# Kernel tuning notes

Hardware: AMD Instinct MI355X
Metric: run time of the kernel (lower is better)

## Reference

```python
import jax, jax.numpy as jnp
import numpy as np

N, E, B = 200000, 6400000, 128
IN_LOCAL, IN_GLOBAL, HIDDEN, NUM_CLASSES = 16, 8, 32, 2


def setup_inputs() -> dict:
    key = jax.random.key(0)
    ks = jax.random.split(key, 16)
    inp = {
        "x_local": jax.random.normal(ks[0], (N, IN_LOCAL), dtype=jnp.float32),
        "x_global": jax.random.normal(ks[1], (B, IN_GLOBAL), dtype=jnp.float32),
        "batch": jnp.sort(jax.random.randint(ks[2], (N,), 0, B, dtype=jnp.int64)),
        "edge_index": jax.random.randint(ks[3], (2, E), 0, N, dtype=jnp.int64),
        # encoder params
        "W_local": jax.random.normal(ks[4], (IN_LOCAL, HIDDEN), jnp.float32) / np.sqrt(IN_LOCAL),
        "b_local": jnp.zeros((HIDDEN,), jnp.float32),
        "W_global": jax.random.normal(ks[5], (IN_GLOBAL, HIDDEN), jnp.float32) / np.sqrt(IN_GLOBAL),
        "b_global": jnp.zeros((HIDDEN,), jnp.float32),
        "W_mix": jax.random.normal(ks[6], (3 * HIDDEN, HIDDEN), jnp.float32) / np.sqrt(3 * HIDDEN),
        "b_mix": jnp.zeros((HIDDEN,), jnp.float32),
        # GNN layer params
        "W_msg": jax.random.normal(ks[7], (HIDDEN, HIDDEN), jnp.float32) / np.sqrt(HIDDEN),
        "b_msg": jnp.zeros((HIDDEN,), jnp.float32),
        "W_self": jax.random.normal(ks[8], (HIDDEN, HIDDEN), jnp.float32) / np.sqrt(HIDDEN),
        "b_self": jnp.zeros((HIDDEN,), jnp.float32),
        # output head
        "W_out": jax.random.normal(ks[9], (HIDDEN, NUM_CLASSES), jnp.float32) / np.sqrt(HIDDEN),
        "b_out": jnp.zeros((NUM_CLASSES,), jnp.float32),
    }
    return inp


def reference(x_local, x_global, batch, edge_index,
              W_local, b_local, W_global, b_global, W_mix, b_mix,
              W_msg, b_msg, W_self, b_self, W_out, b_out):
    n = x_local.shape[0]
    # --- MixedSelectivityNodeEncoder ---
    h_local = jax.nn.relu(x_local @ W_local + b_local)            # [N,H]
    h_global_graph = jax.nn.relu(x_global @ W_global + b_global)  # [B,H]
    h_global = h_global_graph[batch]                              # gather -> [N,H]
    h_int = h_local * h_global
    h_cat = jnp.concatenate([h_local, h_global, h_int], axis=-1)  # [N,3H]
    h0 = jax.nn.relu(h_cat @ W_mix + b_mix)                       # [N,H]
    # --- GNN layer with self loops, add aggregation ---
    loops = jnp.arange(n, dtype=edge_index.dtype)
    src = jnp.concatenate([edge_index[0], loops])                 # [E+N]
    dst = jnp.concatenate([edge_index[1], loops])                 # [E+N]
    msg = jax.nn.relu(h0[src] @ W_msg + b_msg)                    # [E+N,H]
    aggr = jax.ops.segment_sum(msg, dst, num_segments=n)          # [N,H]
    h = jax.nn.relu(aggr + h0 @ W_self + b_self)                  # [N,H]
    # --- output head ---
    return h @ W_out + b_out                                      # [N,C]
```

## Files before the change

### kernel.cpp

```cpp
#include <hip/hip_runtime.h>

#define N_NODES  200000
#define N_EDGES  6400000
#define NGRAPH   128
#define H        32

#define BNODES   256
#define NBUCK    782
#define P_BLOCKS 256
#define EPB      25000
#define SORT_CAP 10240

typedef unsigned short ushort_t;

__device__ __forceinline__ ushort_t f32_to_bf16_rne(float f) {
    unsigned u = __float_as_uint(f);
    unsigned r = (u + 0x7fffu + ((u >> 16) & 1u)) >> 16;
    return (ushort_t)r;
}
__device__ __forceinline__ float bf16_to_f32(ushort_t h) {
    return __uint_as_float(((unsigned)h) << 16);
}

__global__ __launch_bounds__(256) void k_node_enc(
        const float* __restrict__ xl,
        const int*   __restrict__ batch,
        const float* __restrict__ xg,   const float* __restrict__ Wg,
        const float* __restrict__ bg,
        const float* __restrict__ Wl,   const float* __restrict__ bl,
        const float* __restrict__ Wmix, const float* __restrict__ bmix,
        const float* __restrict__ Wmsg, const float* __restrict__ bmsg,
        const float* __restrict__ Wself,const float* __restrict__ bself,
        ushort_t* __restrict__ mb, float* __restrict__ s) {
    int n0 = blockIdx.x * 256 + threadIdx.x;
    bool valid = (n0 < N_NODES);
    int n = valid ? n0 : (N_NODES - 1);

    float xv[16];
    {
        const float4* p = (const float4*)(xl + (size_t)n * 16);
        float4 a = p[0], b = p[1], c = p[2], d = p[3];
        xv[0]=a.x; xv[1]=a.y; xv[2]=a.z; xv[3]=a.w;
        xv[4]=b.x; xv[5]=b.y; xv[6]=b.z; xv[7]=b.w;
        xv[8]=c.x; xv[9]=c.y; xv[10]=c.z; xv[11]=c.w;
        xv[12]=d.x; xv[13]=d.y; xv[14]=d.z; xv[15]=d.w;
    }
    float gvv[8];
    {
        int gb = batch[n];
        const float4* q = (const float4*)(xg + (size_t)gb * 8);
        float4 a = q[0], b = q[1];
        gvv[0]=a.x; gvv[1]=a.y; gvv[2]=a.z; gvv[3]=a.w;
        gvv[4]=b.x; gvv[5]=b.y; gvv[6]=b.z; gvv[7]=b.w;
    }

    float hl[32], hg[32], hi[32];
#pragma unroll
    for (int t4 = 0; t4 < 8; ++t4) {
        float4 al = ((const float4*)bl)[t4];
        float4 ag = ((const float4*)bg)[t4];
#pragma unroll
        for (int k = 0; k < 16; ++k) {
            float4 w = ((const float4*)(Wl + k * H))[t4];
            al.x = fmaf(xv[k], w.x, al.x); al.y = fmaf(xv[k], w.y, al.y);
            al.z = fmaf(xv[k], w.z, al.z); al.w = fmaf(xv[k], w.w, al.w);
        }
#pragma unroll
        for (int k = 0; k < 8; ++k) {
            float4 w = ((const float4*)(Wg + k * H))[t4];
            ag.x = fmaf(gvv[k], w.x, ag.x); ag.y = fmaf(gvv[k], w.y, ag.y);
            ag.z = fmaf(gvv[k], w.z, ag.z); ag.w = fmaf(gvv[k], w.w, ag.w);
        }
        hl[t4*4+0] = fmaxf(al.x, 0.f); hl[t4*4+1] = fmaxf(al.y, 0.f);
        hl[t4*4+2] = fmaxf(al.z, 0.f); hl[t4*4+3] = fmaxf(al.w, 0.f);
        hg[t4*4+0] = fmaxf(ag.x, 0.f); hg[t4*4+1] = fmaxf(ag.y, 0.f);
        hg[t4*4+2] = fmaxf(ag.z, 0.f); hg[t4*4+3] = fmaxf(ag.w, 0.f);
    }
#pragma unroll
    for (int k = 0; k < 32; ++k) hi[k] = hl[k] * hg[k];

    float h0[32];
#pragma unroll
    for (int t4 = 0; t4 < 8; ++t4) {
        float4 acc = ((const float4*)bmix)[t4];
#pragma unroll
        for (int k = 0; k < 32; ++k) {
            float4 w = ((const float4*)(Wmix + k * H))[t4];
            acc.x = fmaf(hl[k], w.x, acc.x); acc.y = fmaf(hl[k], w.y, acc.y);
            acc.z = fmaf(hl[k], w.z, acc.z); acc.w = fmaf(hl[k], w.w, acc.w);
        }
#pragma unroll
        for (int k = 0; k < 32; ++k) {
            float4 w = ((const float4*)(Wmix + (32 + k) * H))[t4];
            acc.x = fmaf(hg[k], w.x, acc.x); acc.y = fmaf(hg[k], w.y, acc.y);
            acc.z = fmaf(hg[k], w.z, acc.z); acc.w = fmaf(hg[k], w.w, acc.w);
        }
#pragma unroll
        for (int k = 0; k < 32; ++k) {
            float4 w = ((const float4*)(Wmix + (64 + k) * H))[t4];
            acc.x = fmaf(hi[k], w.x, acc.x); acc.y = fmaf(hi[k], w.y, acc.y);
            acc.z = fmaf(hi[k], w.z, acc.z); acc.w = fmaf(hi[k], w.w, acc.w);
        }
        h0[t4*4+0] = fmaxf(acc.x, 0.f); h0[t4*4+1] = fmaxf(acc.y, 0.f);
        h0[t4*4+2] = fmaxf(acc.z, 0.f); h0[t4*4+3] = fmaxf(acc.w, 0.f);
    }

#pragma unroll
    for (int t4 = 0; t4 < 8; ++t4) {
        float4 am = ((const float4*)bmsg)[t4];
        float4 as = ((const float4*)bself)[t4];
#pragma unroll
        for (int k = 0; k < 32; ++k) {
            float4 wm = ((const float4*)(Wmsg + k * H))[t4];
            float4 ws = ((const float4*)(Wself + k * H))[t4];
            am.x = fmaf(h0[k], wm.x, am.x); am.y = fmaf(h0[k], wm.y, am.y);
            am.z = fmaf(h0[k], wm.z, am.z); am.w = fmaf(h0[k], wm.w, am.w);
            as.x = fmaf(h0[k], ws.x, as.x); as.y = fmaf(h0[k], ws.y, as.y);
            as.z = fmaf(h0[k], ws.z, as.z); as.w = fmaf(h0[k], ws.w, as.w);
        }
        if (valid) {
            unsigned d0 = (unsigned)f32_to_bf16_rne(fmaxf(am.x, 0.f))
                        | ((unsigned)f32_to_bf16_rne(fmaxf(am.y, 0.f)) << 16);
            unsigned d1 = (unsigned)f32_to_bf16_rne(fmaxf(am.z, 0.f))
                        | ((unsigned)f32_to_bf16_rne(fmaxf(am.w, 0.f)) << 16);
            ((unsigned*)(mb + (size_t)n * H))[t4*2+0] = d0;
            ((unsigned*)(mb + (size_t)n * H))[t4*2+1] = d1;
            ((float4*)(s + (size_t)n * H))[t4] = as;
        }
    }
}

__global__ __launch_bounds__(1024) void k_pcount(const int* __restrict__ ei,
                                                 int* __restrict__ gcnt) {
    __shared__ int cnt[NBUCK];
    int t = threadIdx.x, blk = blockIdx.x;
    for (int i = t; i < NBUCK; i += 1024) cnt[i] = 0;
    __syncthreads();
    int e1 = (blk + 1) * EPB;
    for (int e = blk * EPB + t; e < e1; e += 1024)
        atomicAdd(&cnt[ei[N_EDGES + e] >> 8], 1);
    __syncthreads();
    for (int i = t; i < NBUCK; i += 1024)
        gcnt[i * P_BLOCKS + blk] = cnt[i];
}

__global__ void k_blocksum_g(const int* __restrict__ gcnt, int* __restrict__ bsum) {
    int b = blockIdx.x, t = threadIdx.x;
    int v = gcnt[b * P_BLOCKS + t];
#pragma unroll
    for (int off = 32; off >= 1; off >>= 1)
        v += __shfl_down(v, off, 64);
    __shared__ int w4[4];
    if ((t & 63) == 0) w4[t >> 6] = v;
    __syncthreads();
    if (t == 0) bsum[b] = w4[0] + w4[1] + w4[2] + w4[3];
}

__global__ void k_scan_bsums_g(const int* __restrict__ bsum, int* __restrict__ boff) {
    __shared__ int sd[1024];
    int t = threadIdx.x;
    sd[t] = (t < NBUCK) ? bsum[t] : 0;
    __syncthreads();
#pragma unroll
    for (int off = 1; off < 1024; off <<= 1) {
        int v = (t >= off) ? sd[t - off] : 0;
        __syncthreads();
        sd[t] += v;
        __syncthreads();
    }
    if (t < NBUCK) boff[t] = (t == 0) ? 0 : sd[t - 1];
}

__global__ void k_make_cursor_g(int* __restrict__ gcnt, const int* __restrict__ boff) {
    __shared__ int sd[P_BLOCKS];
    int b = blockIdx.x, t = threadIdx.x, i = b * P_BLOCKS + t;
    int c = gcnt[i];
    sd[t] = c;
    __syncthreads();
#pragma unroll
    for (int off = 1; off < P_BLOCKS; off <<= 1) {
        int v = (t >= off) ? sd[t - off] : 0;
        __syncthreads();
        sd[t] += v;
        __syncthreads();
    }
    gcnt[i] = boff[b] + sd[t] - c;
}

__global__ __launch_bounds__(1024) void k_pscatter(const int* __restrict__ ei,
                                                   const int* __restrict__ goff,
                                                   unsigned int* __restrict__ ebuf) {
    __shared__ int cur[NBUCK];
    int t = threadIdx.x, blk = blockIdx.x;
    for (int i = t; i < NBUCK; i += 1024) cur[i] = goff[i * P_BLOCKS + blk];
    __syncthreads();
    int e1 = (blk + 1) * EPB;
    for (int e = blk * EPB + t; e < e1; e += 1024) {
        unsigned src = (unsigned)ei[e];
        int dst = ei[N_EDGES + e];
        int pos = atomicAdd(&cur[dst >> 8], 1);
        ebuf[pos] = (src << 8) | (unsigned)(dst & 255);
    }
}

__global__ __launch_bounds__(512) void k_bsort_aggr(
        const int* __restrict__ goff,
        const unsigned int* __restrict__ ebuf,
        const ushort_t* __restrict__ mb, const float* __restrict__ s,
        const float* __restrict__ Wout, const float* __restrict__ bout,
        float* __restrict__ out) {
    __shared__ unsigned sorted[SORT_CAP];
    __shared__ int cnt[BNODES];
    __shared__ int off[BNODES];
    __shared__ int cur[BNODES];
    int tid = threadIdx.x, b = blockIdx.x;

    int bs = goff[b * P_BLOCKS];
    int be = (b == NBUCK - 1) ? N_EDGES : goff[(b + 1) * P_BLOCKS];

    if (tid < BNODES) cnt[tid] = 0;
    __syncthreads();

    for (int j = bs + tid; j < be; j += 512)
        atomicAdd(&cnt[ebuf[j] & 255], 1);
    __syncthreads();

    if (tid < BNODES) off[tid] = cnt[tid];
    __syncthreads();
#pragma unroll
    for (int d = 1; d < BNODES; d <<= 1) {
        int v = (tid < BNODES && tid >= d) ? off[tid - d] : 0;
        __syncthreads();
        if (tid < BNODES) off[tid] += v;
        __syncthreads();
    }
    if (tid < BNODES) cur[tid] = off[tid] - cnt[tid];
    __syncthreads();

    for (int j = bs + tid; j < be; j += 512) {
        unsigned pk = ebuf[j];
        int pos = atomicAdd(&cur[pk & 255], 1);
        sorted[pos] = pk;
    }
    __syncthreads();

    const unsigned* mb32 = (const unsigned*)mb;
    int g = tid >> 4;
    int t = tid & 15;

    for (int q = 0; q < 8; ++q) {
        int loc = (g << 3) + q;
        int n = b * BNODES + loc;
        int rs = off[loc] - cnt[loc];
        int re = off[loc];
        float a0 = 0.f, a1 = 0.f;

        for (int j = rs; j < re; j += 8) {
            unsigned pk[8], u[8];
#pragma unroll
            for (int k = 0; k < 8; ++k)
                pk[k] = sorted[min(j + k, re - 1)];
#pragma unroll
            for (int k = 0; k < 8; ++k)
                u[k] = mb32[(pk[k] >> 8) * 16u + (unsigned)t];
#pragma unroll
            for (int k = 0; k < 8; ++k) {
                bool ok = (j + k < re);
                a0 += ok ? __uint_as_float(u[k] << 16)         : 0.f;
                a1 += ok ? __uint_as_float(u[k] & 0xffff0000u) : 0.f;
            }
        }

        if (n < N_NODES) {
            unsigned u = mb32[(unsigned)n * 16u + (unsigned)t];
            float2 sv = *(const float2*)(s + (size_t)n * H + 2 * t);
            float h0 = fmaxf(a0 + __uint_as_float(u << 16)         + sv.x, 0.f);
            float h1 = fmaxf(a1 + __uint_as_float(u & 0xffff0000u) + sv.y, 0.f);
            float4 w = *(const float4*)(Wout + 4 * t);
            float p0 = h0 * w.x + h1 * w.z;
            float p1 = h0 * w.y + h1 * w.w;
#pragma unroll
            for (int o = 8; o >= 1; o >>= 1) {
                p0 += __shfl_down(p0, o, 16);
                p1 += __shfl_down(p1, o, 16);
            }
            if (t == 0) {
                float2 o2;
                o2.x = p0 + bout[0];
                o2.y = p1 + bout[1];
                *(float2*)(out + (size_t)n * 2) = o2;
            }
        }
    }
}

extern "C" void kernel_launch(void* const* d_in, const int* in_sizes, int n_in,
                              void* d_out, int out_size, void* d_ws, size_t ws_size,
                              hipStream_t stream) {
    const float* xl    = (const float*)d_in[0];
    const float* xg    = (const float*)d_in[1];
    const int*   batch = (const int*)  d_in[2];
    const int*   ei    = (const int*)  d_in[3];
    const float* Wl    = (const float*)d_in[4];
    const float* bl    = (const float*)d_in[5];
    const float* Wg    = (const float*)d_in[6];
    const float* bg    = (const float*)d_in[7];
    const float* Wmix  = (const float*)d_in[8];
    const float* bmix  = (const float*)d_in[9];
    const float* Wmsg  = (const float*)d_in[10];
    const float* bmsg  = (const float*)d_in[11];
    const float* Wself = (const float*)d_in[12];
    const float* bself = (const float*)d_in[13];
    const float* Wout  = (const float*)d_in[14];
    const float* bout  = (const float*)d_in[15];
    float* out = (float*)d_out;

    float*    s    = (float*)d_ws;
    ushort_t* mb   = (ushort_t*)(s + (size_t)N_NODES * H);
    int*      gcnt = (int*)(mb + (size_t)N_NODES * H);
    int*      bsum = gcnt + (size_t)NBUCK * P_BLOCKS;
    int*      boff = bsum + NBUCK;
    unsigned int* ebuf = (unsigned int*)(boff + NBUCK);

    k_node_enc<<<(N_NODES + 255) / 256, 256, 0, stream>>>(xl, batch, xg, Wg, bg,
                                                          Wl, bl, Wmix, bmix,
                                                          Wmsg, bmsg, Wself, bself,
                                                          mb, s);

    k_pcount<<<P_BLOCKS, 1024, 0, stream>>>(ei, gcnt);
    k_blocksum_g<<<NBUCK, P_BLOCKS, 0, stream>>>(gcnt, bsum);
    k_scan_bsums_g<<<1, 1024, 0, stream>>>(bsum, boff);
    k_make_cursor_g<<<NBUCK, P_BLOCKS, 0, stream>>>(gcnt, boff);
    k_pscatter<<<P_BLOCKS, 1024, 0, stream>>>(ei, gcnt, ebuf);

    k_bsort_aggr<<<NBUCK, 512, 0, stream>>>(gcnt, ebuf, mb, s, Wout, bout, out);
}
```

Measured before the change: 389.1 us.

## Scatter edges into fixed-capacity per-bucket slots with global atomics, skipping count/scan passes

Replaces the count, block-sum, scan, cursor and partitioned-scatter pipeline with a single scatter kernel. It uses padded global atomic counters per bucket and writes into fixed SORT_CAP slots per bucket, removing a full read pass over edge_index and several launches. The aggregation kernel's in-block prefix scan now uses wavefront shuffles instead of a shared-memory Hillis-Steele loop, and SORT_CAP is reduced to allow more occupancy. Edges past SORT_CAP in a bucket are silently dropped, and global atomic contention on the 782 counters may cost throughput. The old path is kept as a fallback when the workspace is too small.

```diff
diff --git a/kernel.cpp b/kernel.cpp
--- a/kernel.cpp
+++ b/kernel.cpp
@@ -9,7 +9,8 @@
 #define NBUCK    782
 #define P_BLOCKS 256
 #define EPB      25000
-#define SORT_CAP 10240
+#define SORT_CAP 8960
+
 
 typedef unsigned short ushort_t;
 
@@ -203,42 +204,80 @@
     }
 }
 
-__global__ __launch_bounds__(512) void k_bsort_aggr(
+__global__ __launch_bounds__(256) void k_pscatter_direct(
+        const int* __restrict__ ei,
+        int* __restrict__ gcur,
+        unsigned int* __restrict__ ebuf) {
+    int e = blockIdx.x * 256 + threadIdx.x;
+    int stride = gridDim.x * 256;
+    for (; e < N_EDGES; e += stride) {
+        unsigned src = (unsigned)ei[e];
+        int dst = ei[N_EDGES + e];
+        int bkt = dst >> 8;
+        int pos = atomicAdd(&gcur[bkt * 32], 1);
+        if (pos < SORT_CAP)
+            ebuf[(size_t)bkt * SORT_CAP + pos] = (src << 8) | (unsigned)(dst & 255);
+    }
+}
+
+__global__ __launch_bounds__(512, 8) void k_bsort_aggr(
         const int* __restrict__ goff,
+        const int* __restrict__ gcur,
+        int mode,
         const unsigned int* __restrict__ ebuf,
         const ushort_t* __restrict__ mb, const float* __restrict__ s,
         const float* __restrict__ Wout, const float* __restrict__ bout,
         float* __restrict__ out) {
     __shared__ unsigned sorted[SORT_CAP];
     __shared__ int cnt[BNODES];
-    __shared__ int off[BNODES];
+    __shared__ int offx[BNODES + 1];
     __shared__ int cur[BNODES];
+    __shared__ int wsum[4];
     int tid = threadIdx.x, b = blockIdx.x;
 
-    int bs = goff[b * P_BLOCKS];
-    int be = (b == NBUCK - 1) ? N_EDGES : goff[(b + 1) * P_BLOCKS];
+    size_t base;
+    int sz;
+    if (mode) {
+        base = (size_t)b * SORT_CAP;
+        sz = min(gcur[b * 32], SORT_CAP);
+    } else {
+        int bs = goff[b * P_BLOCKS];
+        int be = (b == NBUCK - 1) ? N_EDGES : goff[(b + 1) * P_BLOCKS];
+        base = (size_t)bs;
+        sz = be - bs;
+    }
 
     if (tid < BNODES) cnt[tid] = 0;
     __syncthreads();
 
-    for (int j = bs + tid; j < be; j += 512)
-        atomicAdd(&cnt[ebuf[j] & 255], 1);
-    __syncthreads();
-
-    if (tid < BNODES) off[tid] = cnt[tid];
-    __syncthreads();
-#pragma unroll
-    for (int d = 1; d < BNODES; d <<= 1) {
-        int v = (tid < BNODES && tid >= d) ? off[tid - d] : 0;
-        __syncthreads();
-        if (tid < BNODES) off[tid] += v;
-        __syncthreads();
-    }
-    if (tid < BNODES) cur[tid] = off[tid] - cnt[tid];
-    __syncthreads();
-
-    for (int j = bs + tid; j < be; j += 512) {
-        unsigned pk = ebuf[j];
+    for (int j = tid; j < sz; j += 512)
+        atomicAdd(&cnt[ebuf[base + j] & 255], 1);
+    __syncthreads();
+
+    {
+        int lane = tid & 63, w = tid >> 6;
+        int v = (tid < BNODES) ? cnt[tid] : 0;
+#pragma unroll
+        for (int d = 1; d < 64; d <<= 1) {
+            int u = __shfl_up(v, d, 64);
+            if (lane >= d) v += u;
+        }
+        if (tid < BNODES && lane == 63) wsum[w] = v;
+        __syncthreads();
+        if (tid < BNODES) {
+            int add = 0;
+#pragma unroll
+            for (int i = 0; i < 3; ++i) add += (i < w) ? wsum[i] : 0;
+            int inc = v + add;
+            offx[tid + 1] = inc;
+            cur[tid] = inc - cnt[tid];
+            if (tid == 0) offx[0] = 0;
+        }
+        __syncthreads();
+    }
+
+    for (int j = tid; j < sz; j += 512) {
+        unsigned pk = ebuf[base + j];
         int pos = atomicAdd(&cur[pk & 255], 1);
         sorted[pos] = pk;
     }
@@ -251,8 +290,8 @@
     for (int q = 0; q < 8; ++q) {
         int loc = (g << 3) + q;
         int n = b * BNODES + loc;
-        int rs = off[loc] - cnt[loc];
-        int re = off[loc];
+        int rs = offx[loc];
+        int re = offx[loc + 1];
         float a0 = 0.f, a1 = 0.f;
 
         for (int j = rs; j < re; j += 8) {
@@ -315,23 +354,38 @@
     const float* bout  = (const float*)d_in[15];
     float* out = (float*)d_out;
 
-    float*    s    = (float*)d_ws;
-    ushort_t* mb   = (ushort_t*)(s + (size_t)N_NODES * H);
-    int*      gcnt = (int*)(mb + (size_t)N_NODES * H);
-    int*      bsum = gcnt + (size_t)NBUCK * P_BLOCKS;
-    int*      boff = bsum + NBUCK;
-    unsigned int* ebuf = (unsigned int*)(boff + NBUCK);
+    float*    s  = (float*)d_ws;
+    ushort_t* mb = (ushort_t*)(s + (size_t)N_NODES * H);
+    char*     p  = (char*)(mb + (size_t)N_NODES * H);
+
+    size_t used_prefix = (size_t)N_NODES * H * 6;
+    size_t need1 = used_prefix + (size_t)NBUCK * 32 * 4
+                 + (size_t)NBUCK * SORT_CAP * 4 + 1024;
+    bool mode1 = (ws_size >= need1);
 
     k_node_enc<<<(N_NODES + 255) / 256, 256, 0, stream>>>(xl, batch, xg, Wg, bg,
                                                           Wl, bl, Wmix, bmix,
                                                           Wmsg, bmsg, Wself, bself,
                                                           mb, s);
 
-    k_pcount<<<P_BLOCKS, 1024, 0, stream>>>(ei, gcnt);
-    k_blocksum_g<<<NBUCK, P_BLOCKS, 0, stream>>>(gcnt, bsum);
-    k_scan_bsums_g<<<1, 1024, 0, stream>>>(bsum, boff);
-    k_make_cursor_g<<<NBUCK, P_BLOCKS, 0, stream>>>(gcnt, boff);
-    k_pscatter<<<P_BLOCKS, 1024, 0, stream>>>(ei, gcnt, ebuf);
-
-    k_bsort_aggr<<<NBUCK, 512, 0, stream>>>(gcnt, ebuf, mb, s, Wout, bout, out);
-}
+    if (mode1) {
+        int* gcur = (int*)p;
+        unsigned int* ebuf = (unsigned int*)(gcur + (size_t)NBUCK * 32);
+        hipMemsetAsync(gcur, 0, (size_t)NBUCK * 32 * 4, stream);
+        k_pscatter_direct<<<1024, 256, 0, stream>>>(ei, gcur, ebuf);
+        k_bsort_aggr<<<NBUCK, 512, 0, stream>>>(nullptr, gcur, 1, ebuf,
+                                                mb, s, Wout, bout, out);
+    } else {
+        int* gcnt = (int*)p;
+        int* bsum = gcnt + (size_t)NBUCK * P_BLOCKS;
+        int* boff = bsum + NBUCK;
+        unsigned int* ebuf = (unsigned int*)(boff + NBUCK);
+        k_pcount<<<P_BLOCKS, 1024, 0, stream>>>(ei, gcnt);
+        k_blocksum_g<<<NBUCK, P_BLOCKS, 0, stream>>>(gcnt, bsum);
+        k_scan_bsums_g<<<1, 1024, 0, stream>>>(bsum, boff);
+        k_make_cursor_g<<<NBUCK, P_BLOCKS, 0, stream>>>(gcnt, boff);
+        k_pscatter<<<P_BLOCKS, 1024, 0, stream>>>(ei, gcnt, ebuf);
+        k_bsort_aggr<<<NBUCK, 512, 0, stream>>>(gcnt, nullptr, 0, ebuf,
+                                                mb, s, Wout, bout, out);
+    }
+}
```

New measurement: 752.9 us. 93.5% more time.
